# Optimization experiments

Measured on AMD Instinct MI355X. Metric: run time of the kernel, lower is better.

Reference implementation:

```python
import jax, jax.numpy as jnp
import numpy as np

B = 128
D = 256


def _offsets(lengths):
    # complete (exclusive->inclusive) cumsum with leading zero, like fbgemm asynchronous_complete_cumsum
    return jnp.concatenate([jnp.zeros((1,), lengths.dtype), jnp.cumsum(lengths)])


def jagged_concat2(v0, l0, v1, l1):
    # Per-sample concat of two jagged 2D tensors (same batch size B).
    # v0: [sum(l0), D], v1: [sum(l1), D]. Output: [sum(l0)+sum(l1), D].
    out_len = l0 + l1
    off_out = _offsets(out_len)
    off0 = _offsets(l0)
    off1 = _offsets(l1)
    total = v0.shape[0] + v1.shape[0]  # static
    p = jnp.arange(total, dtype=l0.dtype)
    s = jnp.searchsorted(off_out, p, side='right') - 1  # sample id per output row
    pos = p - off_out[s]                                # position within sample
    from0 = pos < l0[s]
    idx0 = jnp.clip(off0[s] + pos, 0, v0.shape[0] - 1)
    idx1 = jnp.clip(off1[s] + pos - l0[s], 0, v1.shape[0] - 1)
    out = jnp.where(from0[:, None], v0[idx0], v1[idx1])
    return out, out_len


def setup_inputs() -> dict:
    key = jax.random.key(0)
    k1, k2, k3, k4 = jax.random.split(key, 4)
    # ragged item lengths alternating 512/1536 -> sum = B*1024 = 131072
    item_lengths = np.where(np.arange(B) % 2 == 0, 512, 1536).astype(np.int32)
    n_items = int(item_lengths.sum())
    return {
        'item_values': jax.random.normal(k1, (n_items, D), dtype=jnp.float32),
        'action_values': jax.random.normal(k2, (n_items, D), dtype=jnp.float32),
        'ctx0_values': jax.random.normal(k3, (B, D), dtype=jnp.float32),
        'ctx1_values': jax.random.normal(k4, (B, D), dtype=jnp.float32),
        'item_lengths': jnp.asarray(item_lengths),
        'ctx0_lengths': jnp.ones((B,), dtype=jnp.int32),
        'ctx1_lengths': jnp.ones((B,), dtype=jnp.int32),
    }


def reference(item_values, action_values, ctx0_values, ctx1_values,
              item_lengths, ctx0_lengths, ctx1_lengths):
    # 1) Interleave item/action per token: cat(dim=1).view(2N, D)
    n = item_values.shape[0]
    seq = jnp.stack([item_values, action_values], axis=1).reshape(2 * n, D)
    seq_len = item_lengths * 2
    # 2) Per-sample concat of contextual features (jagged_2D_tensor_concat)
    ctx_vals, ctx_len = jagged_concat2(ctx0_values, ctx0_lengths, ctx1_values, ctx1_lengths)
    # 3) Per-sample concat [contextual, interleaved sequence]
    out_vals, out_len = jagged_concat2(ctx_vals, ctx_len, seq, seq_len)
    return out_vals, out_len.astype(jnp.int32)
```

## Files before the change

kernel.cpp:

```cpp
#include <hip/hip_runtime.h>

#define D 256
#define MAXB 128


__global__ void build_offsets_kernel(const int* __restrict__ item_len,
                                     const int* __restrict__ c0_len,
                                     const int* __restrict__ c1_len,
                                     int* __restrict__ offs,
                                     float* __restrict__ out_len_tail,
                                     int Bn) {
    __shared__ int s_oo[MAXB + 1];
    __shared__ int s_io[MAXB + 1];
    __shared__ int s_c0[MAXB + 1];
    __shared__ int s_c1[MAXB + 1];
    int t = threadIdx.x;
    int li = 0, l0 = 0, l1 = 0;
    if (t < Bn) {
        li = item_len[t];
        l0 = c0_len[t];
        l1 = c1_len[t];
    }
    if (t == 0) { s_oo[0] = 0; s_io[0] = 0; s_c0[0] = 0; s_c1[0] = 0; }
    if (t < Bn) {
        s_oo[t + 1] = 2 * li + l0 + l1;
        s_io[t + 1] = li;
        s_c0[t + 1] = l0;
        s_c1[t + 1] = l1;
    }
    __syncthreads();
    for (int off = 1; off < Bn; off <<= 1) {
        int a = 0, b = 0, c = 0, d = 0;
        int idx = t + 1;
        bool act = (t < Bn) && (idx > off);
        if (act) {
            a = s_oo[idx - off];
            b = s_io[idx - off];
            c = s_c0[idx - off];
            d = s_c1[idx - off];
        }
        __syncthreads();
        if (act) {
            s_oo[idx] += a;
            s_io[idx] += b;
            s_c0[idx] += c;
            s_c1[idx] += d;
        }
        __syncthreads();
    }
    for (int i = t; i <= Bn; i += blockDim.x) {
        offs[0 * (Bn + 1) + i] = s_oo[i];
        offs[1 * (Bn + 1) + i] = s_io[i];
        offs[2 * (Bn + 1) + i] = s_c0[i];
        offs[3 * (Bn + 1) + i] = s_c1[i];
    }
    if (t < Bn) out_len_tail[t] = (float)(2 * li + l0 + l1);
}

__global__ __launch_bounds__(256) void copy_rows_kernel(
    const float* __restrict__ item, const float* __restrict__ action,
    const float* __restrict__ c0v, const float* __restrict__ c1v,
    const int* __restrict__ offs, float* __restrict__ out,
    int total_rows, int Bn) {
    __shared__ int s_oo[MAXB + 1];
    __shared__ int s_io[MAXB + 1];
    __shared__ int s_c0[MAXB + 1];
    __shared__ int s_c1[MAXB + 1];
    for (int i = threadIdx.x; i <= Bn; i += blockDim.x) {
        s_oo[i] = offs[0 * (Bn + 1) + i];
        s_io[i] = offs[1 * (Bn + 1) + i];
        s_c0[i] = offs[2 * (Bn + 1) + i];
        s_c1[i] = offs[3 * (Bn + 1) + i];
    }
    __syncthreads();

    int wave = threadIdx.x >> 6;
    int lane = threadIdx.x & 63;
    int r = blockIdx.x * 4 + wave;
    if (r >= total_rows) return;

    int lo = 0, hi = Bn;
    while (hi - lo > 1) {
        int mid = (lo + hi) >> 1;
        if (r >= s_oo[mid]) lo = mid; else hi = mid;
    }
    int s = lo;
    int pos = r - s_oo[s];
    int l0c = s_c0[s + 1] - s_c0[s];
    int l1c = s_c1[s + 1] - s_c1[s];

    const float* src;
    if (pos < l0c) {
        src = c0v + (size_t)(s_c0[s] + pos) * D;
    } else if (pos < l0c + l1c) {
        src = c1v + (size_t)(s_c1[s] + pos - l0c) * D;
    } else {
        int q = pos - l0c - l1c;
        int tk = s_io[s] + (q >> 1);
        src = ((q & 1) ? action : item) + (size_t)tk * D;
    }

    float4 v = reinterpret_cast<const float4*>(src)[lane];
    reinterpret_cast<float4*>(out + (size_t)r * D)[lane] = v;
}

extern "C" void kernel_launch(void* const* d_in, const int* in_sizes, int n_in,
                              void* d_out, int out_size, void* d_ws, size_t ws_size,
                              hipStream_t stream) {
    const float* item   = (const float*)d_in[0];
    const float* action = (const float*)d_in[1];
    const float* c0v    = (const float*)d_in[2];
    const float* c1v    = (const float*)d_in[3];
    const int* item_len = (const int*)d_in[4];
    const int* c0_len   = (const int*)d_in[5];
    const int* c1_len   = (const int*)d_in[6];
    float* out = (float*)d_out;

    int Bn = in_sizes[4];
    int total_rows = (out_size - Bn) / D;
    int* offs = (int*)d_ws;

    build_offsets_kernel<<<1, 128, 0, stream>>>(
        item_len, c0_len, c1_len, offs, out + (size_t)total_rows * D, Bn);

    int grid = (total_rows + 3) / 4;
    copy_rows_kernel<<<grid, 256, 0, stream>>>(
        item, action, c0v, c1v, offs, out, total_rows, Bn);
}
```

Measured before the change: 109.6 us.

## Fuse offset scan into a persistent grid-stride row copy kernel

```diff
diff --git a/kernel.cpp b/kernel.cpp
--- a/kernel.cpp
+++ b/kernel.cpp
@@ -3,17 +3,19 @@
 #define D 256
 #define MAXB 128
 
+typedef float f32x4 __attribute__((ext_vector_type(4)));
 
-__global__ void build_offsets_kernel(const int* __restrict__ item_len,
-                                     const int* __restrict__ c0_len,
-                                     const int* __restrict__ c1_len,
-                                     int* __restrict__ offs,
-                                     float* __restrict__ out_len_tail,
-                                     int Bn) {
+__global__ __launch_bounds__(256) void hstu_preproc_fused(
+    const float* __restrict__ item, const float* __restrict__ action,
+    const float* __restrict__ c0v, const float* __restrict__ c1v,
+    const int* __restrict__ item_len, const int* __restrict__ c0_len,
+    const int* __restrict__ c1_len,
+    float* __restrict__ out, int total_rows, int Bn) {
     __shared__ int s_oo[MAXB + 1];
     __shared__ int s_io[MAXB + 1];
     __shared__ int s_c0[MAXB + 1];
     __shared__ int s_c1[MAXB + 1];
+
     int t = threadIdx.x;
     int li = 0, l0 = 0, l1 = 0;
     if (t < Bn) {
@@ -48,60 +50,43 @@
         }
         __syncthreads();
     }
-    for (int i = t; i <= Bn; i += blockDim.x) {
-        offs[0 * (Bn + 1) + i] = s_oo[i];
-        offs[1 * (Bn + 1) + i] = s_io[i];
-        offs[2 * (Bn + 1) + i] = s_c0[i];
-        offs[3 * (Bn + 1) + i] = s_c1[i];
-    }
-    if (t < Bn) out_len_tail[t] = (float)(2 * li + l0 + l1);
-}
 
-__global__ __launch_bounds__(256) void copy_rows_kernel(
-    const float* __restrict__ item, const float* __restrict__ action,
-    const float* __restrict__ c0v, const float* __restrict__ c1v,
-    const int* __restrict__ offs, float* __restrict__ out,
-    int total_rows, int Bn) {
-    __shared__ int s_oo[MAXB + 1];
-    __shared__ int s_io[MAXB + 1];
-    __shared__ int s_c0[MAXB + 1];
-    __shared__ int s_c1[MAXB + 1];
-    for (int i = threadIdx.x; i <= Bn; i += blockDim.x) {
-        s_oo[i] = offs[0 * (Bn + 1) + i];
-        s_io[i] = offs[1 * (Bn + 1) + i];
-        s_c0[i] = offs[2 * (Bn + 1) + i];
-        s_c1[i] = offs[3 * (Bn + 1) + i];
-    }
-    __syncthreads();
-
-    int wave = threadIdx.x >> 6;
-    int lane = threadIdx.x & 63;
-    int r = blockIdx.x * 4 + wave;
-    if (r >= total_rows) return;
-
-    int lo = 0, hi = Bn;
-    while (hi - lo > 1) {
-        int mid = (lo + hi) >> 1;
-        if (r >= s_oo[mid]) lo = mid; else hi = mid;
-    }
-    int s = lo;
-    int pos = r - s_oo[s];
-    int l0c = s_c0[s + 1] - s_c0[s];
-    int l1c = s_c1[s + 1] - s_c1[s];
-
-    const float* src;
-    if (pos < l0c) {
-        src = c0v + (size_t)(s_c0[s] + pos) * D;
-    } else if (pos < l0c + l1c) {
-        src = c1v + (size_t)(s_c1[s] + pos - l0c) * D;
-    } else {
-        int q = pos - l0c - l1c;
-        int tk = s_io[s] + (q >> 1);
-        src = ((q & 1) ? action : item) + (size_t)tk * D;
+    if (blockIdx.x == 0 && t < Bn) {
+        out[(size_t)total_rows * D + t] = (float)(s_oo[t + 1] - s_oo[t]);
     }
 
-    float4 v = reinterpret_cast<const float4*>(src)[lane];
-    reinterpret_cast<float4*>(out + (size_t)r * D)[lane] = v;
+    int wave = t >> 6;
+    int lane = t & 63;
+    int gwave = blockIdx.x * 4 + wave;
+    int nwaves = gridDim.x * 4;
+
+    for (int r = gwave; r < total_rows; r += nwaves) {
+        int lo = 0, hi = Bn;
+        while (hi - lo > 1) {
+            int mid = (lo + hi) >> 1;
+            if (r >= s_oo[mid]) lo = mid; else hi = mid;
+        }
+        int s = lo;
+        int pos = r - s_oo[s];
+        int l0c = s_c0[s + 1] - s_c0[s];
+        int l1c = s_c1[s + 1] - s_c1[s];
+
+        const float* src;
+        if (pos < l0c) {
+            src = c0v + (size_t)(s_c0[s] + pos) * D;
+        } else if (pos < l0c + l1c) {
+            src = c1v + (size_t)(s_c1[s] + pos - l0c) * D;
+        } else {
+            int q = pos - l0c - l1c;
+            int tk = s_io[s] + (q >> 1);
+            src = ((q & 1) ? action : item) + (size_t)tk * D;
+        }
+
+        f32x4 v = __builtin_nontemporal_load(
+            reinterpret_cast<const f32x4*>(src) + lane);
+        __builtin_nontemporal_store(
+            v, reinterpret_cast<f32x4*>(out + (size_t)r * D) + lane);
+    }
 }
 
 extern "C" void kernel_launch(void* const* d_in, const int* in_sizes, int n_in,
@@ -118,12 +103,8 @@
 
     int Bn = in_sizes[4];
     int total_rows = (out_size - Bn) / D;
-    int* offs = (int*)d_ws;
 
-    build_offsets_kernel<<<1, 128, 0, stream>>>(
-        item_len, c0_len, c1_len, offs, out + (size_t)total_rows * D, Bn);
-
-    int grid = (total_rows + 3) / 4;
-    copy_rows_kernel<<<grid, 256, 0, stream>>>(
-        item, action, c0v, c1v, offs, out, total_rows, Bn);
+    int grid = 2048;
+    hstu_preproc_fused<<<grid, 256, 0, stream>>>(
+        item, action, c0v, c1v, item_len, c0_len, c1_len, out, total_rows, Bn);
 }
```

Result: faster. 96.04 us (-12.4%).
